# Optimization experiments

Hardware: AMD Instinct MI355X
Metric: run time of the kernel (lower is better)

## Reference

```python
import jax, jax.numpy as jnp
import numpy as np

B, C_IN, N_NODES = 128, 64, 1024
N_TRIPLES = 3 * (N_NODES - 1)  # node 0 is the shared zero vector


def _btc(x, idx, w, b):
    # x: [B, C, N]; idx: [B, 3M]; w: [O, C, 3]; b: [O]
    Bv, C, _ = x.shape
    T = idx.shape[1]
    g = jnp.take_along_axis(x, jnp.broadcast_to(idx[:, None, :], (Bv, C, T)), axis=2)
    g = g.reshape(Bv, C, T // 3, 3)  # stride-3 kernel-3 conv == per-triple contraction
    out = jnp.einsum('bcnk,ock->bon', g, w) + b[None, :, None]
    zero = jnp.zeros((Bv, out.shape[1], 1), dtype=out.dtype)
    return jnp.concatenate([zero, out], axis=2)  # re-prepend zero node -> [B, O, N]


def _tln(x):
    mean = jnp.mean(x, axis=(1, 2), keepdims=True)
    std = jnp.std(x, axis=(1, 2), ddof=1, keepdims=True)  # torch.std is unbiased
    return (x - mean) / (std + 1e-5)


def _tower(x, idx, p):
    x = jax.nn.leaky_relu(_tln(_btc(x, idx, p['w_conv1'], p['b_conv1'])), 0.01)
    x = jax.nn.leaky_relu(_tln(_btc(x, idx, p['w_conv2'], p['b_conv2'])), 0.01)
    x = _tln(_btc(x, idx, p['w_conv3'], p['b_conv3']))
    x = jnp.max(x, axis=2)  # DynamicPooling -> [B, 64]
    x = jax.nn.leaky_relu(x @ p['w_fc1'].T + p['b_fc1'], 0.01)
    return x @ p['w_fc2'].T + p['b_fc2']  # [B, 1]  (Dropout is identity at eval)


def setup_inputs() -> dict:
    key = jax.random.key(0)
    ks = jax.random.split(key, 12)
    s = 0.05
    return {
        'data1': jax.random.normal(ks[0], (B, C_IN, N_NODES), jnp.float32),
        'idx1': jax.random.randint(ks[1], (B, N_TRIPLES, 1), 0, N_NODES, dtype=jnp.int64)
                if jax.config.jax_enable_x64 else
                jax.random.randint(ks[1], (B, N_TRIPLES, 1), 0, N_NODES).astype(jnp.int32),
        'data2': jax.random.normal(ks[2], (B, C_IN, N_NODES), jnp.float32),
        'idx2': jax.random.randint(ks[3], (B, N_TRIPLES, 1), 0, N_NODES).astype(jnp.int32),
        'w_conv1': jax.random.normal(ks[4], (256, C_IN, 3), jnp.float32) * s,
        'b_conv1': jnp.zeros((256,), jnp.float32),
        'w_conv2': jax.random.normal(ks[5], (128, 256, 3), jnp.float32) * s,
        'b_conv2': jnp.zeros((128,), jnp.float32),
        'w_conv3': jax.random.normal(ks[6], (64, 128, 3), jnp.float32) * s,
        'b_conv3': jnp.zeros((64,), jnp.float32),
        'w_fc1': jax.random.normal(ks[7], (32, 64), jnp.float32) * s,
        'b_fc1': jnp.zeros((32,), jnp.float32),
        'w_fc2': jax.random.normal(ks[8], (1, 32), jnp.float32) * s,
        'b_fc2': jnp.zeros((1,), jnp.float32),
    }


def reference(data1, idx1, data2, idx2,
              w_conv1, b_conv1, w_conv2, b_conv2, w_conv3, b_conv3,
              w_fc1, b_fc1, w_fc2, b_fc2):
    p = dict(w_conv1=w_conv1, b_conv1=b_conv1, w_conv2=w_conv2, b_conv2=b_conv2,
             w_conv3=w_conv3, b_conv3=b_conv3, w_fc1=w_fc1, b_fc1=b_fc1,
             w_fc2=w_fc2, b_fc2=b_fc2)
    y1 = _tower(data1, idx1[..., 0], p)
    y2 = _tower(data2, idx2[..., 0], p)
    return jnp.squeeze(jax.nn.sigmoid(y1 - y2), axis=1)  # [B]
```

## Files before the change

### kernel.cpp

```cpp
#include <hip/hip_runtime.h>
#include <math.h>

typedef __attribute__((ext_vector_type(8))) short short8;
typedef __attribute__((ext_vector_type(4))) float f32x4;
typedef __attribute__((ext_vector_type(2))) float f32x2;

#define LRELU(x) ((x) > 0.0f ? (x) : 0.01f * (x))

struct __align__(4) Int3 { int x, y, z; };

__device__ __forceinline__ unsigned short f2bf(float f) {
    unsigned int u = __float_as_uint(f);
    return (unsigned short)((u + 0x7FFFu + ((u >> 16) & 1u)) >> 16);
}
__device__ __forceinline__ unsigned int pack_bf16_pair(float lo, float hi) {
    unsigned int ul = __float_as_uint(lo) + 0x8000u;
    unsigned int uh = __float_as_uint(hi) + 0x8000u;
    return (ul >> 16) | (uh & 0xFFFF0000u);
}
__device__ __forceinline__ float2 stats_from(const float* sums, int b, float count) {
    float s = sums[2 * b], q = sums[2 * b + 1];
    float mean = s / count;
    float var = (q - s * s / count) / (count - 1.0f);
    var = fmaxf(var, 0.0f);
    return make_float2(mean, 1.0f / (sqrtf(var) + 1e-5f));
}
__device__ __forceinline__ void atomicMaxF(float* a, float v) {
    if (v >= 0.0f) atomicMax((int*)a, __float_as_int(v));
    else           atomicMin((unsigned int*)a, __float_as_uint(v));
}
__device__ __forceinline__ unsigned int fp8x4_nact(unsigned int u, float a, float c) {
    f32x2 lo = __builtin_amdgcn_cvt_pk_f32_fp8(u, false);
    f32x2 hi = __builtin_amdgcn_cvt_pk_f32_fp8(u, true);
    lo = lo * a + c; hi = hi * a + c;
    f32x2 ml = lo * 0.01f, mh = hi * 0.01f;
    lo = __builtin_elementwise_max(lo, ml);
    hi = __builtin_elementwise_max(hi, mh);
    int r = __builtin_amdgcn_cvt_pk_fp8_f32(lo.x, lo.y, 0, false);
    r = __builtin_amdgcn_cvt_pk_fp8_f32(hi.x, hi.y, r, true);
    return (unsigned int)r;
}
__device__ __forceinline__ int perm128(int o) {
    return ((o >> 6) << 6) | (((o >> 3) & 3) << 4) | (((o >> 5) & 1) << 3) | (o & 7);
}

template <int MT, int WM>
__device__ __forceinline__ void mfma_step(const unsigned short* wt, const unsigned short* gt,
                                          f32x4 (&acc)[MT][4],
                                          int wo, int wn, int quad, int l15, int blkid)
{
#pragma unroll
    for (int st = 0; st < 2; ++st) {
        short8 af[MT], bfv[4];
        const int qb = st * 4 + quad;
#pragma unroll
        for (int i = 0; i < MT; i++) {
            const int orow = wo * WM + i * 16 + l15;
            af[i] = *(const short8*)&wt[orow * 64 + ((qb ^ blkid) << 3)];
        }
#pragma unroll
        for (int t = 0; t < 4; t++) {
            const int nrow = wn * 64 + t * 16 + l15;
            bfv[t] = *(const short8*)&gt[nrow * 64 + ((qb ^ blkid) << 3)];
        }
#pragma unroll
        for (int i = 0; i < MT; i++)
#pragma unroll
            for (int t = 0; t < 4; t++)
                acc[i][t] = __builtin_amdgcn_mfma_f32_16x16x32_bf16(
                    af[i], bfv[t], acc[i][t], 0, 0, 0);
    }
}

__global__ void prep_all(const float* __restrict__ w1, unsigned short* __restrict__ wq1,
                         const float* __restrict__ w2, unsigned char* __restrict__ wq2,
                         const float* __restrict__ w3, unsigned char* __restrict__ wq3)
{
    const int tid = blockIdx.x * blockDim.x + threadIdx.x;
    const int stride = gridDim.x * blockDim.x;
    for (int i = tid; i < 256 * 192; i += stride) {
        int o = i / 192, kp = i - o * 192;
        int j = kp >> 6, c = kp & 63;
        wq1[i] = f2bf(w1[(o * 64 + c) * 3 + j]);
    }
    for (int i = tid; i < (128 * 768) >> 2; i += stride) {
        const int e0 = i << 2;
        const int o = e0 / 768, r0 = e0 - o * 768;
        const int kc = r0 >> 7, ro = r0 & 127;
        const int k0 = ((ro >> 6) << 6) + (((ro >> 3) & 1) << 5) + (((ro >> 4) & 3) << 3) + (ro & 7);
        const int kp0 = kc * 128 + k0;
        const int j = kp0 >> 8, c0 = kp0 & 255;
        const float* src = &w2[(o * 256 + c0) * 3 + j];
        float f0 = src[0], f1 = src[3], f2 = src[6], f3 = src[9];
        int r = __builtin_amdgcn_cvt_pk_fp8_f32(f0, f1, 0, false);
        r = __builtin_amdgcn_cvt_pk_fp8_f32(f2, f3, r, true);
        *(unsigned int*)&wq2[e0] = (unsigned int)r;
    }
    for (int i = tid; i < (64 * 384) >> 2; i += stride) {
        const int e0 = i << 2;
        const int o = e0 / 384, r0 = e0 - o * 384;
        const int kc = r0 >> 7, ro = r0 & 127;
        const int k0 = ((ro >> 6) << 6) + (((ro >> 3) & 1) << 5) + (((ro >> 4) & 3) << 3) + (ro & 7);
        const int kp0 = kc * 128 + k0;
        const int j = kp0 >> 7, c0 = kp0 & 127;
        const float* src = &w3[(o * 128 + c0) * 3 + j];
        float f0 = src[0], f1 = src[3], f2 = src[6], f3 = src[9];
        int r = __builtin_amdgcn_cvt_pk_fp8_f32(f0, f1, 0, false);
        r = __builtin_amdgcn_cvt_pk_fp8_f32(f2, f3, r, true);
        *(unsigned int*)&wq3[e0] = (unsigned int)r;
    }
}

__global__ __launch_bounds__(256) void transpose_in(const float* __restrict__ inA,
                                                    const float* __restrict__ inB,
                                                    unsigned short* __restrict__ xT,
                                                    float* __restrict__ sums,
                                                    unsigned int* __restrict__ pmax)
{
    const int b = blockIdx.y, n0 = blockIdx.x * 64;
    const float* in = (b >= 128 ? inB : inA) + ((size_t)(b & 127) * 64) * 1024;
    const int tid = threadIdx.x;
    if (blockIdx.x == 0 && blockIdx.y == 0) {
        const int nBv = gridDim.y;
        for (int i = tid; i < 3 * nBv * 2; i += 256) sums[i] = 0.0f;
        for (int i = tid; i < nBv * 64; i += 256) pmax[i] = 0xFFFFFFFFu;
    }
    __shared__ float tile[64][65];
    const int nn = tid & 63, cw = tid >> 6;
#pragma unroll
    for (int i = 0; i < 16; i++) {
        int c = i * 4 + cw;
        tile[c][nn] = in[(size_t)c * 1024 + n0 + nn];
    }
    __syncthreads();
    const int n = tid >> 2, cp = (tid & 3) * 16;
    unsigned int pk[8];
#pragma unroll
    for (int i = 0; i < 8; i++) {
        unsigned short lo = f2bf(tile[cp + 2 * i][n]);
        unsigned short hi = f2bf(tile[cp + 2 * i + 1][n]);
        pk[i] = (unsigned int)lo | ((unsigned int)hi << 16);
    }
    unsigned short* dst = xT + ((size_t)b * 1024 + n0 + n) * 64 + cp;
    uint4 v0 = {pk[0], pk[1], pk[2], pk[3]};
    uint4 v1 = {pk[4], pk[5], pk[6], pk[7]};
    *(uint4*)dst = v0;
    *(uint4*)(dst + 8) = v1;
}

__global__ __launch_bounds__(256) void norm_act_fp8(unsigned char* __restrict__ a,
                                                    const float* __restrict__ sums,
                                                    float count, int u4PerB)
{
    const int b = blockIdx.y;
    float2 st = stats_from(sums, b, count);
    const float na = st.y, nc = -st.x * st.y;
    uint4* p = (uint4*)a + (size_t)b * u4PerB;
    for (int idx = blockIdx.x * 256 + threadIdx.x; idx < u4PerB; idx += gridDim.x * 256) {
        uint4 v = p[idx];
        v.x = fp8x4_nact(v.x, na, nc);
        v.y = fp8x4_nact(v.y, na, nc);
        v.z = fp8x4_nact(v.z, na, nc);
        v.w = fp8x4_nact(v.w, na, nc);
        p[idx] = v;
    }
}

__global__ __launch_bounds__(256, 3) void conv1_mfma(
    const unsigned short* __restrict__ xT,
    const int* __restrict__ idxA,
    const int* __restrict__ idxB,
    const unsigned short* __restrict__ wq,
    const float* __restrict__ bias,
    unsigned char* __restrict__ out,
    float* __restrict__ sums)
{
    const int b   = blockIdx.x;
    const int o0  = blockIdx.y * 128;
    const int nt0 = blockIdx.z << 7;
    const int tid = threadIdx.x;
    const int lane = tid & 63, wave = tid >> 6;
    const int wo = wave & 1, wn = wave >> 1;
    const int quad = lane >> 4, l15 = lane & 15;
    const int blkid = lane & 7;

    __shared__ __align__(16) unsigned short wt[128 * 64];
    __shared__ __align__(16) unsigned short gt[128 * 64];

    f32x4 acc[4][4];
#pragma unroll
    for (int i = 0; i < 4; i++)
#pragma unroll
        for (int t = 0; t < 4; t++) acc[i][t] = (f32x4){0.f, 0.f, 0.f, 0.f};

    const unsigned short* xTb = xT + (((size_t)b) << 10) * 64;
    const int* idxb = (b >= 128 ? idxB : idxA) + (size_t)(b & 127) * 3069;

    const int gr = tid >> 1, gh = tid & 1;
    int s0, s1, s2;
    {
        int n = nt0 + gr;
        int t0 = (n == 0) ? 0 : (n - 1);
        const Int3 sv = *(const Int3*)&idxb[3 * t0];
        s0 = sv.x; s1 = sv.y; s2 = sv.z;
    }
    const int wr = tid >> 1, wseg = tid & 1;
    const unsigned short* wrow = wq + (size_t)(o0 + wr) * 192 + wseg * 32;
    const int gswz = gr & 7, wswz = wr & 7;

    uint4 g0A, g1A, g2A, g3A;
    uint4 g0B, g1B, g2B, g3B;

#define LOADC(S, KC) {                                                           \
        const int src_ = ((KC) == 0) ? s0 : (((KC) == 1) ? s1 : s2);             \
        const uint4* gp_ = (const uint4*)(xTb + (size_t)src_ * 64 + gh * 32);    \
        g0##S = gp_[0]; g1##S = gp_[1]; g2##S = gp_[2]; g3##S = gp_[3];          \
    }

#define STAGE(S, KC) {                                                           \
        const uint4* wp_ = (const uint4*)(wrow + ((KC) << 6));                   \
        uint4 wv0 = wp_[0], wv1 = wp_[1], wv2 = wp_[2], wv3 = wp_[3];            \
        *(uint4*)&gt[gr * 64 + (((gh << 2) | 0) ^ gswz) * 8] = g0##S;            \
        *(uint4*)&gt[gr * 64 + (((gh << 2) | 1) ^ gswz) * 8] = g1##S;            \
        *(uint4*)&gt[gr * 64 + (((gh << 2) | 2) ^ gswz) * 8] = g2##S;            \
        *(uint4*)&gt[gr * 64 + (((gh << 2) | 3) ^ gswz) * 8] = g3##S;            \
        *(uint4*)&wt[wr * 64 + ((wseg * 4 + 0) ^ wswz) * 8] = wv0;               \
        *(uint4*)&wt[wr * 64 + ((wseg * 4 + 1) ^ wswz) * 8] = wv1;               \
        *(uint4*)&wt[wr * 64 + ((wseg * 4 + 2) ^ wswz) * 8] = wv2;               \
        *(uint4*)&wt[wr * 64 + ((wseg * 4 + 3) ^ wswz) * 8] = wv3;               \
    }

    LOADC(A, 0);
    LOADC(B, 1);
    int kc = 0;
    for (; kc + 2 <= 3; kc += 2) {
        if (kc) __syncthreads();
        STAGE(A, kc);
        if (kc + 2 < 3) LOADC(A, kc + 2);
        __syncthreads();
        mfma_step<4, 64>(wt, gt, acc, wo, wn, quad, l15, blkid);
        __syncthreads();
        STAGE(B, kc + 1);
        __syncthreads();
        mfma_step<4, 64>(wt, gt, acc, wo, wn, quad, l15, blkid);
    }
    {
        __syncthreads();
        STAGE(A, 2);
        __syncthreads();
        mfma_step<4, 64>(wt, gt, acc, wo, wn, quad, l15, blkid);
    }
#undef LOADC
#undef STAGE

    __syncthreads();
    unsigned char* eb = (unsigned char*)gt;
    float lsum = 0.f, lsq = 0.f;
#pragma unroll
    for (int i = 0; i < 4; i++) {
        const int obl = wo * 64 + i * 16 + quad * 4;
        const int op  = perm128(obl);
        const float4 bv = *(const float4*)(bias + o0 + obl);
#pragma unroll
        for (int t = 0; t < 4; t++) {
            const int nl = wn * 64 + t * 16 + l15;
            float v0 = acc[i][t][0] + bv.x;
            float v1 = acc[i][t][1] + bv.y;
            float v2 = acc[i][t][2] + bv.z;
            float v3 = acc[i][t][3] + bv.w;
            if (nt0 + nl == 0) { v0 = v1 = v2 = v3 = 0.f; }
            lsum += v0 + v1 + v2 + v3;
            lsq  += v0 * v0 + v1 * v1 + v2 * v2 + v3 * v3;
            int r = __builtin_amdgcn_cvt_pk_fp8_f32(v0, v1, 0, false);
            r = __builtin_amdgcn_cvt_pk_fp8_f32(v2, v3, r, true);
            *(unsigned int*)&eb[nl * 128 + (op ^ ((nl & 7) << 4))] = (unsigned int)r;
        }
    }
#pragma unroll
    for (int off = 32; off > 0; off >>= 1) {
        lsum += __shfl_down(lsum, off);
        lsq  += __shfl_down(lsq, off);
    }
    float* red = (float*)wt;
    if (lane == 0) { red[wave] = lsum; red[4 + wave] = lsq; }
    __syncthreads();
#pragma unroll
    for (int c = 0; c < 4; ++c) {
        const int ch = c * 256 + tid;
        const int row = ch >> 3, off = (ch & 7) << 4;
        uint4 v = *(const uint4*)&eb[row * 128 + (off ^ ((row & 7) << 4))];
        *(uint4*)&out[((size_t)b * 1024 + nt0 + row) * 256 + o0 + off] = v;
    }
    if (tid == 0) {
        atomicAdd(&sums[2 * b + 0], red[0] + red[1] + red[2] + red[3]);
        atomicAdd(&sums[2 * b + 1], red[4] + red[5] + red[6] + red[7]);
    }
}

__global__ __launch_bounds__(256, 3) void conv2_fp8(
    const unsigned char* __restrict__ a1,
    const int* __restrict__ idxA,
    const int* __restrict__ idxB,
    const unsigned char* __restrict__ wq8,
    const float* __restrict__ bias,
    unsigned char* __restrict__ out,
    float* __restrict__ sums)
{
    const int b   = blockIdx.x;
    const int nt0 = blockIdx.z << 7;
    const int tid = threadIdx.x;
    const int lane = tid & 63, wave = tid >> 6;
    const int wo = wave & 1, wn = wave >> 1;
    const int quad = lane >> 4, l15 = lane & 15;
    const int blkid = lane & 7;

    __shared__ __align__(16) unsigned char wt8[128 * 128];
    __shared__ __align__(16) unsigned char gt8[128 * 128];

    f32x4 acc[4][4];
#pragma unroll
    for (int i = 0; i < 4; i++)
#pragma unroll
        for (int t = 0; t < 4; t++) acc[i][t] = (f32x4){0.f, 0.f, 0.f, 0.f};

    const unsigned char* xb = a1 + (((size_t)b) << 10) * 256;
    const int* idxb = (b >= 128 ? idxB : idxA) + (size_t)(b & 127) * 3069;

    const int gr = tid >> 1, gh = tid & 1;
    int si0, si1, si2;
    {
        int n = nt0 + gr;
        int t0 = (n == 0) ? 0 : (n - 1);
        const Int3 sv = *(const Int3*)&idxb[3 * t0];
        si0 = sv.x; si1 = sv.y; si2 = sv.z;
    }
    const unsigned char* wrow = wq8 + (size_t)gr * 768 + gh * 64;
    const int swz = gr & 7;

    uint4 g0A, g1A, g2A, g3A;
    uint4 g0B, g1B, g2B, g3B;

#define LOADC2(S, KC) {                                                          \
        const int j_  = (KC) >> 1;                                               \
        const int c0_ = ((KC) & 1) << 7;                                         \
        const int src_ = (j_ == 0) ? si0 : ((j_ == 1) ? si1 : si2);              \
        const uint4* gp_ = (const uint4*)(xb + (size_t)src_ * 256 + c0_ + gh * 64); \
        g0##S = gp_[0]; g1##S = gp_[1]; g2##S = gp_[2]; g3##S = gp_[3];          \
    }

#define STAGE2(S, KC) {                                                          \
        const uint4* wp_ = (const uint4*)(wrow + (KC) * 128);                    \
        uint4 wv0 = wp_[0], wv1 = wp_[1], wv2 = wp_[2], wv3 = wp_[3];            \
        *(uint4*)&gt8[gr * 128 + (((gh << 2) | 0) ^ swz) * 16] = g0##S;          \
        *(uint4*)&gt8[gr * 128 + (((gh << 2) | 1) ^ swz) * 16] = g1##S;          \
        *(uint4*)&gt8[gr * 128 + (((gh << 2) | 2) ^ swz) * 16] = g2##S;          \
        *(uint4*)&gt8[gr * 128 + (((gh << 2) | 3) ^ swz) * 16] = g3##S;          \
        *(uint4*)&wt8[gr * 128 + (((gh << 2) | 0) ^ swz) * 16] = wv0;            \
        *(uint4*)&wt8[gr * 128 + (((gh << 2) | 1) ^ swz) * 16] = wv1;            \
        *(uint4*)&wt8[gr * 128 + (((gh << 2) | 2) ^ swz) * 16] = wv2;            \
        *(uint4*)&wt8[gr * 128 + (((gh << 2) | 3) ^ swz) * 16] = wv3;            \
    }

#define MFMA_STEP2 {                                                             \
        _Pragma("unroll")                                                        \
        for (int pp = 0; pp < 2; ++pp) {                                         \
            ulonglong2 a0v, a1v, a2v, a3v, b0v, b1v, b2v, b3v;                   \
            {                                                                    \
                const int cx = (((pp * 4 + quad) ^ blkid) << 4);                 \
                a0v = *(const ulonglong2*)&wt8[(wo * 64 +  0 + l15) * 128 + cx]; \
                a1v = *(const ulonglong2*)&wt8[(wo * 64 + 16 + l15) * 128 + cx]; \
                a2v = *(const ulonglong2*)&wt8[(wo * 64 + 32 + l15) * 128 + cx]; \
                a3v = *(const ulonglong2*)&wt8[(wo * 64 + 48 + l15) * 128 + cx]; \
                b0v = *(const ulonglong2*)&gt8[(wn * 64 +  0 + l15) * 128 + cx]; \
                b1v = *(const ulonglong2*)&gt8[(wn * 64 + 16 + l15) * 128 + cx]; \
                b2v = *(const ulonglong2*)&gt8[(wn * 64 + 32 + l15) * 128 + cx]; \
                b3v = *(const ulonglong2*)&gt8[(wn * 64 + 48 + l15) * 128 + cx]; \
            }                                                                    \
            acc[0][0] = __builtin_amdgcn_mfma_f32_16x16x32_fp8_fp8((long)a0v.x, (long)b0v.x, acc[0][0], 0, 0, 0); \
            acc[0][1] = __builtin_amdgcn_mfma_f32_16x16x32_fp8_fp8((long)a0v.x, (long)b1v.x, acc[0][1], 0, 0, 0); \
            acc[0][2] = __builtin_amdgcn_mfma_f32_16x16x32_fp8_fp8((long)a0v.x, (long)b2v.x, acc[0][2], 0, 0, 0); \
            acc[0][3] = __builtin_amdgcn_mfma_f32_16x16x32_fp8_fp8((long)a0v.x, (long)b3v.x, acc[0][3], 0, 0, 0); \
            acc[1][0] = __builtin_amdgcn_mfma_f32_16x16x32_fp8_fp8((long)a1v.x, (long)b0v.x, acc[1][0], 0, 0, 0); \
            acc[1][1] = __builtin_amdgcn_mfma_f32_16x16x32_fp8_fp8((long)a1v.x, (long)b1v.x, acc[1][1], 0, 0, 0); \
            acc[1][2] = __builtin_amdgcn_mfma_f32_16x16x32_fp8_fp8((long)a1v.x, (long)b2v.x, acc[1][2], 0, 0, 0); \
            acc[1][3] = __builtin_amdgcn_mfma_f32_16x16x32_fp8_fp8((long)a1v.x, (long)b3v.x, acc[1][3], 0, 0, 0); \
            acc[2][0] = __builtin_amdgcn_mfma_f32_16x16x32_fp8_fp8((long)a2v.x, (long)b0v.x, acc[2][0], 0, 0, 0); \
            acc[2][1] = __builtin_amdgcn_mfma_f32_16x16x32_fp8_fp8((long)a2v.x, (long)b1v.x, acc[2][1], 0, 0, 0); \
            acc[2][2] = __builtin_amdgcn_mfma_f32_16x16x32_fp8_fp8((long)a2v.x, (long)b2v.x, acc[2][2], 0, 0, 0); \
            acc[2][3] = __builtin_amdgcn_mfma_f32_16x16x32_fp8_fp8((long)a2v.x, (long)b3v.x, acc[2][3], 0, 0, 0); \
            acc[3][0] = __builtin_amdgcn_mfma_f32_16x16x32_fp8_fp8((long)a3v.x, (long)b0v.x, acc[3][0], 0, 0, 0); \
            acc[3][1] = __builtin_amdgcn_mfma_f32_16x16x32_fp8_fp8((long)a3v.x, (long)b1v.x, acc[3][1], 0, 0, 0); \
            acc[3][2] = __builtin_amdgcn_mfma_f32_16x16x32_fp8_fp8((long)a3v.x, (long)b2v.x, acc[3][2], 0, 0, 0); \
            acc[3][3] = __builtin_amdgcn_mfma_f32_16x16x32_fp8_fp8((long)a3v.x, (long)b3v.x, acc[3][3], 0, 0, 0); \
            acc[0][0] = __builtin_amdgcn_mfma_f32_16x16x32_fp8_fp8((long)a0v.y, (long)b0v.y, acc[0][0], 0, 0, 0); \
            acc[0][1] = __builtin_amdgcn_mfma_f32_16x16x32_fp8_fp8((long)a0v.y, (long)b1v.y, acc[0][1], 0, 0, 0); \
            acc[0][2] = __builtin_amdgcn_mfma_f32_16x16x32_fp8_fp8((long)a0v.y, (long)b2v.y, acc[0][2], 0, 0, 0); \
            acc[0][3] = __builtin_amdgcn_mfma_f32_16x16x32_fp8_fp8((long)a0v.y, (long)b3v.y, acc[0][3], 0, 0, 0); \
            acc[1][0] = __builtin_amdgcn_mfma_f32_16x16x32_fp8_fp8((long)a1v.y, (long)b0v.y, acc[1][0], 0, 0, 0); \
            acc[1][1] = __builtin_amdgcn_mfma_f32_16x16x32_fp8_fp8((long)a1v.y, (long)b1v.y, acc[1][1], 0, 0, 0); \
            acc[1][2] = __builtin_amdgcn_mfma_f32_16x16x32_fp8_fp8((long)a1v.y, (long)b2v.y, acc[1][2], 0, 0, 0); \
            acc[1][3] = __builtin_amdgcn_mfma_f32_16x16x32_fp8_fp8((long)a1v.y, (long)b3v.y, acc[1][3], 0, 0, 0); \
            acc[2][0] = __builtin_amdgcn_mfma_f32_16x16x32_fp8_fp8((long)a2v.y, (long)b0v.y, acc[2][0], 0, 0, 0); \
            acc[2][1] = __builtin_amdgcn_mfma_f32_16x16x32_fp8_fp8((long)a2v.y, (long)b1v.y, acc[2][1], 0, 0, 0); \
            acc[2][2] = __builtin_amdgcn_mfma_f32_16x16x32_fp8_fp8((long)a2v.y, (long)b2v.y, acc[2][2], 0, 0, 0); \
            acc[2][3] = __builtin_amdgcn_mfma_f32_16x16x32_fp8_fp8((long)a2v.y, (long)b3v.y, acc[2][3], 0, 0, 0); \
            acc[3][0] = __builtin_amdgcn_mfma_f32_16x16x32_fp8_fp8((long)a3v.y, (long)b0v.y, acc[3][0], 0, 0, 0); \
            acc[3][1] = __builtin_amdgcn_mfma_f32_16x16x32_fp8_fp8((long)a3v.y, (long)b1v.y, acc[3][1], 0, 0, 0); \
            acc[3][2] = __builtin_amdgcn_mfma_f32_16x16x32_fp8_fp8((long)a3v.y, (long)b2v.y, acc[3][2], 0, 0, 0); \
            acc[3][3] = __builtin_amdgcn_mfma_f32_16x16x32_fp8_fp8((long)a3v.y, (long)b3v.y, acc[3][3], 0, 0, 0); \
        }                                                                        \
    }

    LOADC2(A, 0);
    LOADC2(B, 1);
    int kc = 0;
    for (; kc + 2 <= 6; kc += 2) {
        if (kc) __syncthreads();
        STAGE2(A, kc);
        if (kc + 2 < 6) LOADC2(A, kc + 2);
        __syncthreads();
        MFMA_STEP2;
        __syncthreads();
        STAGE2(B, kc + 1);
        if (kc + 3 < 6) LOADC2(B, kc + 3);
        __syncthreads();
        MFMA_STEP2;
    }
#undef LOADC2
#undef STAGE2
#undef MFMA_STEP2

    __syncthreads();
    unsigned char* eb = gt8;
    float lsum = 0.f, lsq = 0.f;
#pragma unroll
    for (int i = 0; i < 4; i++) {
        const int obl = wo * 64 + i * 16 + quad * 4;
        const int op  = perm128(obl);
        const float4 bv = *(const float4*)(bias + obl);
#pragma unroll
        for (int t = 0; t < 4; t++) {
            const int nl = wn * 64 + t * 16 + l15;
            float v0 = acc[i][t][0] + bv.x;
            float v1 = acc[i][t][1] + bv.y;
            float v2 = acc[i][t][2] + bv.z;
            float v3 = acc[i][t][3] + bv.w;
            if (nt0 + nl == 0) { v0 = v1 = v2 = v3 = 0.f; }
            lsum += v0 + v1 + v2 + v3;
            lsq  += v0 * v0 + v1 * v1 + v2 * v2 + v3 * v3;
            int r = __builtin_amdgcn_cvt_pk_fp8_f32(v0, v1, 0, false);
            r = __builtin_amdgcn_cvt_pk_fp8_f32(v2, v3, r, true);
            *(unsigned int*)&eb[nl * 128 + (op ^ ((nl & 7) << 4))] = (unsigned int)r;
        }
    }
#pragma unroll
    for (int off = 32; off > 0; off >>= 1) {
        lsum += __shfl_down(lsum, off);
        lsq  += __shfl_down(lsq, off);
    }
    float* red = (float*)wt8;
    if (lane == 0) { red[wave] = lsum; red[4 + wave] = lsq; }
    __syncthreads();
#pragma unroll
    for (int c = 0; c < 4; ++c) {
        const int ch = c * 256 + tid;
        const int row = ch >> 3, off = (ch & 7) << 4;
        uint4 v = *(const uint4*)&eb[row * 128 + (off ^ ((row & 7) << 4))];
        *(uint4*)&out[((size_t)b * 1024 + nt0 + row) * 128 + off] = v;
    }
    if (tid == 0) {
        atomicAdd(&sums[2 * b + 0], red[0] + red[1] + red[2] + red[3]);
        atomicAdd(&sums[2 * b + 1], red[4] + red[5] + red[6] + red[7]);
    }
}

__global__ __launch_bounds__(256, 3) void conv3_fp8(
    const unsigned char* __restrict__ a2,
    const int* __restrict__ idxA,
    const int* __restrict__ idxB,
    const unsigned char* __restrict__ wq8,
    const float* __restrict__ bias,
    float* __restrict__ sums,
    float* __restrict__ pmax)
{
    const int b   = blockIdx.x;
    const int nt0 = blockIdx.z << 7;
    const int tid = threadIdx.x;
    const int lane = tid & 63, wave = tid >> 6;
    const int wo = wave & 1, wn = wave >> 1;
    const int quad = lane >> 4, l15 = lane & 15;
    const int blkid = lane & 7;

    __shared__ __align__(16) unsigned char wt8[64 * 128];
    __shared__ __align__(16) unsigned char gt8[128 * 128];

    f32x4 acc[2][4];
#pragma unroll
    for (int i = 0; i < 2; i++)
#pragma unroll
        for (int t = 0; t < 4; t++) acc[i][t] = (f32x4){0.f, 0.f, 0.f, 0.f};

    const unsigned char* xb = a2 + (((size_t)b) << 10) * 128;
    const int* idxb = (b >= 128 ? idxB : idxA) + (size_t)(b & 127) * 3069;

    const int gr = tid >> 1, gh = tid & 1;
    int si0, si1, si2;
    {
        int n = nt0 + gr;
        int t0 = (n == 0) ? 0 : (n - 1);
        const Int3 sv = *(const Int3*)&idxb[3 * t0];
        si0 = sv.x; si1 = sv.y; si2 = sv.z;
    }
    const int wr = tid >> 2, wseg = tid & 3;
    const unsigned char* wrow = wq8 + (size_t)wr * 384 + wseg * 32;
    const int gswz = gr & 7, wswz = wr & 7;

    uint4 g0A, g1A, g2A, g3A;
    uint4 g0B, g1B, g2B, g3B;

#define LOADC3(S, KC) {                                                          \
        const int src_ = ((KC) == 0) ? si0 : (((KC) == 1) ? si1 : si2);          \
        const uint4* gp_ = (const uint4*)(xb + (size_t)src_ * 128 + gh * 64);    \
        g0##S = gp_[0]; g1##S = gp_[1]; g2##S = gp_[2]; g3##S = gp_[3];          \
    }

#define STAGE3(S, KC) {                                                          \
        const uint4* wp_ = (const uint4*)(wrow + (KC) * 128);                    \
        uint4 wv0 = wp_[0], wv1 = wp_[1];                                        \
        *(uint4*)&gt8[gr * 128 + (((gh << 2) | 0) ^ gswz) * 16] = g0##S;         \
        *(uint4*)&gt8[gr * 128 + (((gh << 2) | 1) ^ gswz) * 16] = g1##S;         \
        *(uint4*)&gt8[gr * 128 + (((gh << 2) | 2) ^ gswz) * 16] = g2##S;         \
        *(uint4*)&gt8[gr * 128 + (((gh << 2) | 3) ^ gswz) * 16] = g3##S;         \
        *(uint4*)&wt8[wr * 128 + (((wseg << 1) | 0) ^ wswz) * 16] = wv0;         \
        *(uint4*)&wt8[wr * 128 + (((wseg << 1) | 1) ^ wswz) * 16] = wv1;         \
    }

#define MFMA_STEP3 {                                                             \
        _Pragma("unroll")                                                        \
        for (int pp = 0; pp < 2; ++pp) {                                         \
            ulonglong2 a0v, a1v, b0v, b1v, b2v, b3v;                             \
            {                                                                    \
                const int cx = (((pp * 4 + quad) ^ blkid) << 4);                 \
                a0v = *(const ulonglong2*)&wt8[(wo * 32 +  0 + l15) * 128 + cx]; \
                a1v = *(const ulonglong2*)&wt8[(wo * 32 + 16 + l15) * 128 + cx]; \
                b0v = *(const ulonglong2*)&gt8[(wn * 64 +  0 + l15) * 128 + cx]; \
                b1v = *(const ulonglong2*)&gt8[(wn * 64 + 16 + l15) * 128 + cx]; \
                b2v = *(const ulonglong2*)&gt8[(wn * 64 + 32 + l15) * 128 + cx]; \
                b3v = *(const ulonglong2*)&gt8[(wn * 64 + 48 + l15) * 128 + cx]; \
            }                                                                    \
            acc[0][0] = __builtin_amdgcn_mfma_f32_16x16x32_fp8_fp8((long)a0v.x, (long)b0v.x, acc[0][0], 0, 0, 0); \
            acc[0][1] = __builtin_amdgcn_mfma_f32_16x16x32_fp8_fp8((long)a0v.x, (long)b1v.x, acc[0][1], 0, 0, 0); \
            acc[0][2] = __builtin_amdgcn_mfma_f32_16x16x32_fp8_fp8((long)a0v.x, (long)b2v.x, acc[0][2], 0, 0, 0); \
            acc[0][3] = __builtin_amdgcn_mfma_f32_16x16x32_fp8_fp8((long)a0v.x, (long)b3v.x, acc[0][3], 0, 0, 0); \
            acc[1][0] = __builtin_amdgcn_mfma_f32_16x16x32_fp8_fp8((long)a1v.x, (long)b0v.x, acc[1][0], 0, 0, 0); \
            acc[1][1] = __builtin_amdgcn_mfma_f32_16x16x32_fp8_fp8((long)a1v.x, (long)b1v.x, acc[1][1], 0, 0, 0); \
            acc[1][2] = __builtin_amdgcn_mfma_f32_16x16x32_fp8_fp8((long)a1v.x, (long)b2v.x, acc[1][2], 0, 0, 0); \
            acc[1][3] = __builtin_amdgcn_mfma_f32_16x16x32_fp8_fp8((long)a1v.x, (long)b3v.x, acc[1][3], 0, 0, 0); \
            acc[0][0] = __builtin_amdgcn_mfma_f32_16x16x32_fp8_fp8((long)a0v.y, (long)b0v.y, acc[0][0], 0, 0, 0); \
            acc[0][1] = __builtin_amdgcn_mfma_f32_16x16x32_fp8_fp8((long)a0v.y, (long)b1v.y, acc[0][1], 0, 0, 0); \
            acc[0][2] = __builtin_amdgcn_mfma_f32_16x16x32_fp8_fp8((long)a0v.y, (long)b2v.y, acc[0][2], 0, 0, 0); \
            acc[0][3] = __builtin_amdgcn_mfma_f32_16x16x32_fp8_fp8((long)a0v.y, (long)b3v.y, acc[0][3], 0, 0, 0); \
            acc[1][0] = __builtin_amdgcn_mfma_f32_16x16x32_fp8_fp8((long)a1v.y, (long)b0v.y, acc[1][0], 0, 0, 0); \
            acc[1][1] = __builtin_amdgcn_mfma_f32_16x16x32_fp8_fp8((long)a1v.y, (long)b1v.y, acc[1][1], 0, 0, 0); \
            acc[1][2] = __builtin_amdgcn_mfma_f32_16x16x32_fp8_fp8((long)a1v.y, (long)b2v.y, acc[1][2], 0, 0, 0); \
            acc[1][3] = __builtin_amdgcn_mfma_f32_16x16x32_fp8_fp8((long)a1v.y, (long)b3v.y, acc[1][3], 0, 0, 0); \
        }                                                                        \
    }

    LOADC3(A, 0);
    LOADC3(B, 1);
    int kc = 0;
    for (; kc + 2 <= 3; kc += 2) {
        if (kc) __syncthreads();
        STAGE3(A, kc);
        if (kc + 2 < 3) LOADC3(A, kc + 2);
        __syncthreads();
        MFMA_STEP3;
        __syncthreads();
        STAGE3(B, kc + 1);
        __syncthreads();
        MFMA_STEP3;
    }
    {
        __syncthreads();
        STAGE3(A, 2);
        __syncthreads();
        MFMA_STEP3;
    }
#undef LOADC3
#undef STAGE3
#undef MFMA_STEP3

    __syncthreads();
    float lsum = 0.f, lsq = 0.f;
#pragma unroll
    for (int i = 0; i < 2; i++) {
        const int ob = wo * 32 + i * 16 + quad * 4;
        const float4 bv = *(const float4*)(bias + ob);
        float mx0 = -1e30f, mx1 = -1e30f, mx2 = -1e30f, mx3 = -1e30f;
#pragma unroll
        for (int t = 0; t < 4; t++) {
            const int n = nt0 + wn * 64 + t * 16 + l15;
            float v0 = acc[i][t][0] + bv.x;
            float v1 = acc[i][t][1] + bv.y;
            float v2 = acc[i][t][2] + bv.z;
            float v3 = acc[i][t][3] + bv.w;
            if (n == 0) { v0 = v1 = v2 = v3 = 0.f; }
            lsum += v0 + v1 + v2 + v3;
            lsq  += v0 * v0 + v1 * v1 + v2 * v2 + v3 * v3;
            mx0 = fmaxf(mx0, v0); mx1 = fmaxf(mx1, v1);
            mx2 = fmaxf(mx2, v2); mx3 = fmaxf(mx3, v3);
        }
#pragma unroll
        for (int off = 1; off < 16; off <<= 1) {
            mx0 = fmaxf(mx0, __shfl_xor(mx0, off));
            mx1 = fmaxf(mx1, __shfl_xor(mx1, off));
            mx2 = fmaxf(mx2, __shfl_xor(mx2, off));
            mx3 = fmaxf(mx3, __shfl_xor(mx3, off));
        }
        if (l15 == 0) {
            atomicMaxF(&pmax[(size_t)b * 64 + ob + 0], mx0);
            atomicMaxF(&pmax[(size_t)b * 64 + ob + 1], mx1);
            atomicMaxF(&pmax[(size_t)b * 64 + ob + 2], mx2);
            atomicMaxF(&pmax[(size_t)b * 64 + ob + 3], mx3);
        }
    }
#pragma unroll
    for (int off = 32; off > 0; off >>= 1) {
        lsum += __shfl_down(lsum, off);
        lsq  += __shfl_down(lsq, off);
    }
    float* red = (float*)wt8;
    if (lane == 0) { red[wave] = lsum; red[4 + wave] = lsq; }
    __syncthreads();
    if (tid == 0) {
        atomicAdd(&sums[2 * b + 0], red[0] + red[1] + red[2] + red[3]);
        atomicAdd(&sums[2 * b + 1], red[4] + red[5] + red[6] + red[7]);
    }
}

__global__ __launch_bounds__(64) void fc_head(
    const float* __restrict__ pmax, const float* __restrict__ sums3, float count,
    const float* __restrict__ w_fc1, const float* __restrict__ b_fc1,
    const float* __restrict__ w_fc2, const float* __restrict__ b_fc2,
    float* __restrict__ y)
{
    const int b = blockIdx.x, t = threadIdx.x;
    __shared__ float pooled[64];
    __shared__ float hid[32];
    float2 s = stats_from(sums3, b, count);
    pooled[t] = (pmax[(size_t)b * 64 + t] - s.x) * s.y;
    __syncthreads();
    if (t < 32) {
        float h = b_fc1[t];
#pragma unroll
        for (int c = 0; c < 64; c++) h += pooled[c] * w_fc1[t * 64 + c];
        hid[t] = LRELU(h);
    }
    __syncthreads();
    if (t == 0) {
        float v = b_fc2[0];
#pragma unroll
        for (int c = 0; c < 32; c++) v += hid[c] * w_fc2[c];
        y[b] = v;
    }
}

__global__ void sigmoid_diff(const float* __restrict__ y1,
                             const float* __restrict__ y2,
                             float* __restrict__ out)
{
    int b = threadIdx.x;
    if (b < 128) out[b] = 1.0f / (1.0f + expf(-(y1[b] - y2[b])));
}

extern "C" void kernel_launch(void* const* d_in, const int* in_sizes, int n_in,
                              void* d_out, int out_size, void* d_ws, size_t ws_size,
                              hipStream_t stream)
{
    const float* data1 = (const float*)d_in[0];
    const int*   idx1  = (const int*)d_in[1];
    const float* data2 = (const float*)d_in[2];
    const int*   idx2  = (const int*)d_in[3];
    const float* w1 = (const float*)d_in[4];
    const float* b1 = (const float*)d_in[5];
    const float* w2 = (const float*)d_in[6];
    const float* b2 = (const float*)d_in[7];
    const float* w3 = (const float*)d_in[8];
    const float* b3 = (const float*)d_in[9];
    const float* wfc1 = (const float*)d_in[10];
    const float* bfc1 = (const float*)d_in[11];
    const float* wfc2 = (const float*)d_in[12];
    const float* bfc2 = (const float*)d_in[13];

    const size_t needM = (size_t)256 * 1024 * (64 * 2 + 256 * 1 + 128 * 1) + 768 * 1024;
    const bool merged = ws_size >= needM;
    const int nB = merged ? 256 : 128;
    const size_t szXT = (size_t)nB * 1024 * 64 * 2;
    const size_t szA1 = (size_t)nB * 1024 * 256;
    const size_t szA2 = (size_t)nB * 1024 * 128;

    char* ws = (char*)d_ws;
    unsigned short* xT = (unsigned short*)ws;
    unsigned char*  a1 = (unsigned char*)(ws + szXT);
    unsigned char*  a2 = (unsigned char*)(ws + szXT + szA1);
    char* tail = ws + szXT + szA1 + szA2;
    unsigned short* wq1   = (unsigned short*)tail;
    unsigned char*  wq2f8 = (unsigned char*)(tail + 128 * 1024);
    unsigned char*  wq3f8 = (unsigned char*)(tail + 384 * 1024);
    float* sums = (float*)(tail + 448 * 1024);
    float* pmax = (float*)(tail + 512 * 1024);
    float* yv   = (float*)(tail + 640 * 1024);

    prep_all<<<96, 256, 0, stream>>>(w1, wq1, w2, wq2f8, w3, wq3f8);

    const int nIter = merged ? 1 : 2;
    for (int t = 0; t < nIter; ++t) {
        const float* dA = (merged || t == 0) ? data1 : data2;
        const float* dB = merged ? data2 : dA;
        const int* iA = (merged || t == 0) ? idx1 : idx2;
        const int* iB = merged ? idx2 : iA;
        float* s1 = sums;
        float* s2 = sums + nB * 2;
        float* s3 = sums + nB * 4;

        transpose_in<<<dim3(16, nB), 256, 0, stream>>>(dA, dB, xT, sums,
                                                       (unsigned int*)pmax);

        conv1_mfma<<<dim3(nB, 2, 8), 256, 0, stream>>>(
            xT, iA, iB, wq1, b1, a1, s1);

        norm_act_fp8<<<dim3(16, nB), 256, 0, stream>>>(a1, s1, 256.0f * 1024.0f, 16384);

        conv2_fp8<<<dim3(nB, 1, 8), 256, 0, stream>>>(
            a1, iA, iB, wq2f8, b2, a2, s2);

        norm_act_fp8<<<dim3(8, nB), 256, 0, stream>>>(a2, s2, 128.0f * 1024.0f, 8192);

        conv3_fp8<<<dim3(nB, 1, 8), 256, 0, stream>>>(
            a2, iA, iB, wq3f8, b3, s3, pmax);

        fc_head<<<nB, 64, 0, stream>>>(pmax, s3, 64.0f * 1024.0f,
                                       wfc1, bfc1, wfc2, bfc2,
                                       yv + (merged ? 0 : t * 128));
    }
    sigmoid_diff<<<1, 128, 0, stream>>>(yv, yv + 128, (float*)d_out);
}
```

Baseline: 269.5 us.

## Enlarge conv workgroups to 512 threads with bigger output tiles

All three conv kernels now run 8-wave, 512-thread blocks. conv1 covers all 256 output channels per block instead of splitting across blockIdx.y, so each gathered input tile is loaded once. conv2 and conv3 now cover 256 nodes per block instead of 128, so each weight tile is reused over twice as many nodes. The aim is to cut redundant gather and weight traffic and block count, at the cost of more LDS per block, fewer blocks (less parallelism for small grids) and reworked staging and epilogue index maps.

```diff
diff --git a/kernel.cpp b/kernel.cpp
--- a/kernel.cpp
+++ b/kernel.cpp
@@ -166,7 +166,7 @@
     }
 }
 
-__global__ __launch_bounds__(256, 3) void conv1_mfma(
+__global__ __launch_bounds__(512, 2) void conv1_mfma(
     const unsigned short* __restrict__ xT,
     const int* __restrict__ idxA,
     const int* __restrict__ idxB,
@@ -176,15 +176,14 @@
     float* __restrict__ sums)
 {
     const int b   = blockIdx.x;
-    const int o0  = blockIdx.y * 128;
     const int nt0 = blockIdx.z << 7;
     const int tid = threadIdx.x;
     const int lane = tid & 63, wave = tid >> 6;
-    const int wo = wave & 1, wn = wave >> 1;
+    const int wo = wave & 3, wn = wave >> 2;
     const int quad = lane >> 4, l15 = lane & 15;
     const int blkid = lane & 7;
 
-    __shared__ __align__(16) unsigned short wt[128 * 64];
+    __shared__ __align__(16) unsigned short wt[256 * 64];
     __shared__ __align__(16) unsigned short gt[128 * 64];
 
     f32x4 acc[4][4];
@@ -196,7 +195,7 @@
     const unsigned short* xTb = xT + (((size_t)b) << 10) * 64;
     const int* idxb = (b >= 128 ? idxB : idxA) + (size_t)(b & 127) * 3069;
 
-    const int gr = tid >> 1, gh = tid & 1;
+    const int gr = tid >> 2, gh = tid & 3;
     int s0, s1, s2;
     {
         int n = nt0 + gr;
@@ -205,25 +204,22 @@
         s0 = sv.x; s1 = sv.y; s2 = sv.z;
     }
     const int wr = tid >> 1, wseg = tid & 1;
-    const unsigned short* wrow = wq + (size_t)(o0 + wr) * 192 + wseg * 32;
+    const unsigned short* wrow = wq + (size_t)wr * 192 + wseg * 32;
     const int gswz = gr & 7, wswz = wr & 7;
 
-    uint4 g0A, g1A, g2A, g3A;
-    uint4 g0B, g1B, g2B, g3B;
+    uint4 g0A, g1A, g0B, g1B;
 
 #define LOADC(S, KC) {                                                           \
         const int src_ = ((KC) == 0) ? s0 : (((KC) == 1) ? s1 : s2);             \
-        const uint4* gp_ = (const uint4*)(xTb + (size_t)src_ * 64 + gh * 32);    \
-        g0##S = gp_[0]; g1##S = gp_[1]; g2##S = gp_[2]; g3##S = gp_[3];          \
+        const uint4* gp_ = (const uint4*)(xTb + (size_t)src_ * 64 + gh * 16);    \
+        g0##S = gp_[0]; g1##S = gp_[1];                                          \
     }
 
 #define STAGE(S, KC) {                                                           \
         const uint4* wp_ = (const uint4*)(wrow + ((KC) << 6));                   \
         uint4 wv0 = wp_[0], wv1 = wp_[1], wv2 = wp_[2], wv3 = wp_[3];            \
-        *(uint4*)&gt[gr * 64 + (((gh << 2) | 0) ^ gswz) * 8] = g0##S;            \
-        *(uint4*)&gt[gr * 64 + (((gh << 2) | 1) ^ gswz) * 8] = g1##S;            \
-        *(uint4*)&gt[gr * 64 + (((gh << 2) | 2) ^ gswz) * 8] = g2##S;            \
-        *(uint4*)&gt[gr * 64 + (((gh << 2) | 3) ^ gswz) * 8] = g3##S;            \
+        *(uint4*)&gt[gr * 64 + (((gh << 1) | 0) ^ gswz) * 8] = g0##S;            \
+        *(uint4*)&gt[gr * 64 + (((gh << 1) | 1) ^ gswz) * 8] = g1##S;            \
         *(uint4*)&wt[wr * 64 + ((wseg * 4 + 0) ^ wswz) * 8] = wv0;               \
         *(uint4*)&wt[wr * 64 + ((wseg * 4 + 1) ^ wswz) * 8] = wv1;               \
         *(uint4*)&wt[wr * 64 + ((wseg * 4 + 2) ^ wswz) * 8] = wv2;               \
@@ -254,13 +250,13 @@
 #undef STAGE
 
     __syncthreads();
-    unsigned char* eb = (unsigned char*)gt;
+    unsigned char* eb = (unsigned char*)wt;
     float lsum = 0.f, lsq = 0.f;
 #pragma unroll
     for (int i = 0; i < 4; i++) {
         const int obl = wo * 64 + i * 16 + quad * 4;
         const int op  = perm128(obl);
-        const float4 bv = *(const float4*)(bias + o0 + obl);
+        const float4 bv = *(const float4*)(bias + obl);
 #pragma unroll
         for (int t = 0; t < 4; t++) {
             const int nl = wn * 64 + t * 16 + l15;
@@ -273,7 +269,7 @@
             lsq  += v0 * v0 + v1 * v1 + v2 * v2 + v3 * v3;
             int r = __builtin_amdgcn_cvt_pk_fp8_f32(v0, v1, 0, false);
             r = __builtin_amdgcn_cvt_pk_fp8_f32(v2, v3, r, true);
-            *(unsigned int*)&eb[nl * 128 + (op ^ ((nl & 7) << 4))] = (unsigned int)r;
+            *(unsigned int*)&eb[nl * 256 + (op ^ ((nl & 7) << 4))] = (unsigned int)r;
         }
     }
 #pragma unroll
@@ -281,23 +277,28 @@
         lsum += __shfl_down(lsum, off);
         lsq  += __shfl_down(lsq, off);
     }
-    float* red = (float*)wt;
-    if (lane == 0) { red[wave] = lsum; red[4 + wave] = lsq; }
-    __syncthreads();
-#pragma unroll
-    for (int c = 0; c < 4; ++c) {
-        const int ch = c * 256 + tid;
-        const int row = ch >> 3, off = (ch & 7) << 4;
-        uint4 v = *(const uint4*)&eb[row * 128 + (off ^ ((row & 7) << 4))];
-        *(uint4*)&out[((size_t)b * 1024 + nt0 + row) * 256 + o0 + off] = v;
+    float* red = (float*)gt;
+    if (lane == 0) { red[wave] = lsum; red[8 + wave] = lsq; }
+    __syncthreads();
+    {
+        const int row = tid >> 2, c0 = (tid & 3) * 64;
+#pragma unroll
+        for (int i = 0; i < 4; ++i) {
+            const int off = c0 + i * 16;
+            uint4 v = *(const uint4*)&eb[row * 256 + (off ^ ((row & 7) << 4))];
+            *(uint4*)&out[((size_t)b * 1024 + nt0 + row) * 256 + off] = v;
+        }
     }
     if (tid == 0) {
-        atomicAdd(&sums[2 * b + 0], red[0] + red[1] + red[2] + red[3]);
-        atomicAdd(&sums[2 * b + 1], red[4] + red[5] + red[6] + red[7]);
-    }
-}
-
-__global__ __launch_bounds__(256, 3) void conv2_fp8(
+        float a0 = 0.f, a1 = 0.f;
+#pragma unroll
+        for (int w = 0; w < 8; ++w) { a0 += red[w]; a1 += red[8 + w]; }
+        atomicAdd(&sums[2 * b + 0], a0);
+        atomicAdd(&sums[2 * b + 1], a1);
+    }
+}
+
+__global__ __launch_bounds__(512, 2) void conv2_fp8(
     const unsigned char* __restrict__ a1,
     const int* __restrict__ idxA,
     const int* __restrict__ idxB,
@@ -307,7 +308,7 @@
     float* __restrict__ sums)
 {
     const int b   = blockIdx.x;
-    const int nt0 = blockIdx.z << 7;
+    const int nt0 = blockIdx.z << 8;
     const int tid = threadIdx.x;
     const int lane = tid & 63, wave = tid >> 6;
     const int wo = wave & 1, wn = wave >> 1;
@@ -315,7 +316,7 @@
     const int blkid = lane & 7;
 
     __shared__ __align__(16) unsigned char wt8[128 * 128];
-    __shared__ __align__(16) unsigned char gt8[128 * 128];
+    __shared__ __align__(16) unsigned char gt8[256 * 128];
 
     f32x4 acc[4][4];
 #pragma unroll
@@ -334,8 +335,9 @@
         const Int3 sv = *(const Int3*)&idxb[3 * t0];
         si0 = sv.x; si1 = sv.y; si2 = sv.z;
     }
-    const unsigned char* wrow = wq8 + (size_t)gr * 768 + gh * 64;
-    const int swz = gr & 7;
+    const int wr = tid >> 2, wseg = tid & 3;
+    const unsigned char* wrow = wq8 + (size_t)wr * 768 + wseg * 32;
+    const int gswz = gr & 7, wswz = wr & 7;
 
     uint4 g0A, g1A, g2A, g3A;
     uint4 g0B, g1B, g2B, g3B;
@@ -350,15 +352,13 @@
 
 #define STAGE2(S, KC) {                                                          \
         const uint4* wp_ = (const uint4*)(wrow + (KC) * 128);                    \
-        uint4 wv0 = wp_[0], wv1 = wp_[1], wv2 = wp_[2], wv3 = wp_[3];            \
-        *(uint4*)&gt8[gr * 128 + (((gh << 2) | 0) ^ swz) * 16] = g0##S;          \
-        *(uint4*)&gt8[gr * 128 + (((gh << 2) | 1) ^ swz) * 16] = g1##S;          \
-        *(uint4*)&gt8[gr * 128 + (((gh << 2) | 2) ^ swz) * 16] = g2##S;          \
-        *(uint4*)&gt8[gr * 128 + (((gh << 2) | 3) ^ swz) * 16] = g3##S;          \
-        *(uint4*)&wt8[gr * 128 + (((gh << 2) | 0) ^ swz) * 16] = wv0;            \
-        *(uint4*)&wt8[gr * 128 + (((gh << 2) | 1) ^ swz) * 16] = wv1;            \
-        *(uint4*)&wt8[gr * 128 + (((gh << 2) | 2) ^ swz) * 16] = wv2;            \
-        *(uint4*)&wt8[gr * 128 + (((gh << 2) | 3) ^ swz) * 16] = wv3;            \
+        uint4 wv0 = wp_[0], wv1 = wp_[1];                                        \
+        *(uint4*)&gt8[gr * 128 + (((gh << 2) | 0) ^ gswz) * 16] = g0##S;         \
+        *(uint4*)&gt8[gr * 128 + (((gh << 2) | 1) ^ gswz) * 16] = g1##S;         \
+        *(uint4*)&gt8[gr * 128 + (((gh << 2) | 2) ^ gswz) * 16] = g2##S;         \
+        *(uint4*)&gt8[gr * 128 + (((gh << 2) | 3) ^ gswz) * 16] = g3##S;         \
+        *(uint4*)&wt8[wr * 128 + (((wseg << 1) | 0) ^ wswz) * 16] = wv0;         \
+        *(uint4*)&wt8[wr * 128 + (((wseg << 1) | 1) ^ wswz) * 16] = wv1;         \
     }
 
 #define MFMA_STEP2 {                                                             \
@@ -459,22 +459,27 @@
         lsq  += __shfl_down(lsq, off);
     }
     float* red = (float*)wt8;
-    if (lane == 0) { red[wave] = lsum; red[4 + wave] = lsq; }
-    __syncthreads();
-#pragma unroll
-    for (int c = 0; c < 4; ++c) {
-        const int ch = c * 256 + tid;
-        const int row = ch >> 3, off = (ch & 7) << 4;
-        uint4 v = *(const uint4*)&eb[row * 128 + (off ^ ((row & 7) << 4))];
-        *(uint4*)&out[((size_t)b * 1024 + nt0 + row) * 128 + off] = v;
+    if (lane == 0) { red[wave] = lsum; red[8 + wave] = lsq; }
+    __syncthreads();
+    {
+        const int row = tid >> 1, c0 = (tid & 1) * 64;
+#pragma unroll
+        for (int i = 0; i < 4; ++i) {
+            const int off = c0 + i * 16;
+            uint4 v = *(const uint4*)&eb[row * 128 + (off ^ ((row & 7) << 4))];
+            *(uint4*)&out[((size_t)b * 1024 + nt0 + row) * 128 + off] = v;
+        }
     }
     if (tid == 0) {
-        atomicAdd(&sums[2 * b + 0], red[0] + red[1] + red[2] + red[3]);
-        atomicAdd(&sums[2 * b + 1], red[4] + red[5] + red[6] + red[7]);
-    }
-}
-
-__global__ __launch_bounds__(256, 3) void conv3_fp8(
+        float a0 = 0.f, a1v = 0.f;
+#pragma unroll
+        for (int w = 0; w < 8; ++w) { a0 += red[w]; a1v += red[8 + w]; }
+        atomicAdd(&sums[2 * b + 0], a0);
+        atomicAdd(&sums[2 * b + 1], a1v);
+    }
+}
+
+__global__ __launch_bounds__(512, 2) void conv3_fp8(
     const unsigned char* __restrict__ a2,
     const int* __restrict__ idxA,
     const int* __restrict__ idxB,
@@ -484,7 +489,7 @@
     float* __restrict__ pmax)
 {
     const int b   = blockIdx.x;
-    const int nt0 = blockIdx.z << 7;
+    const int nt0 = blockIdx.z << 8;
     const int tid = threadIdx.x;
     const int lane = tid & 63, wave = tid >> 6;
     const int wo = wave & 1, wn = wave >> 1;
@@ -492,7 +497,7 @@
     const int blkid = lane & 7;
 
     __shared__ __align__(16) unsigned char wt8[64 * 128];
-    __shared__ __align__(16) unsigned char gt8[128 * 128];
+    __shared__ __align__(16) unsigned char gt8[256 * 128];
 
     f32x4 acc[2][4];
 #pragma unroll
@@ -511,8 +516,8 @@
         const Int3 sv = *(const Int3*)&idxb[3 * t0];
         si0 = sv.x; si1 = sv.y; si2 = sv.z;
     }
-    const int wr = tid >> 2, wseg = tid & 3;
-    const unsigned char* wrow = wq8 + (size_t)wr * 384 + wseg * 32;
+    const int wr = tid >> 3, wseg = tid & 7;
+    const unsigned char* wrow = wq8 + (size_t)wr * 384 + wseg * 16;
     const int gswz = gr & 7, wswz = wr & 7;
 
     uint4 g0A, g1A, g2A, g3A;
@@ -525,14 +530,12 @@
     }
 
 #define STAGE3(S, KC) {                                                          \
-        const uint4* wp_ = (const uint4*)(wrow + (KC) * 128);                    \
-        uint4 wv0 = wp_[0], wv1 = wp_[1];                                        \
+        uint4 wv0 = *(const uint4*)(wrow + (KC) * 128);                          \
         *(uint4*)&gt8[gr * 128 + (((gh << 2) | 0) ^ gswz) * 16] = g0##S;         \
         *(uint4*)&gt8[gr * 128 + (((gh << 2) | 1) ^ gswz) * 16] = g1##S;         \
         *(uint4*)&gt8[gr * 128 + (((gh << 2) | 2) ^ gswz) * 16] = g2##S;         \
         *(uint4*)&gt8[gr * 128 + (((gh << 2) | 3) ^ gswz) * 16] = g3##S;         \
-        *(uint4*)&wt8[wr * 128 + (((wseg << 1) | 0) ^ wswz) * 16] = wv0;         \
-        *(uint4*)&wt8[wr * 128 + (((wseg << 1) | 1) ^ wswz) * 16] = wv1;         \
+        *(uint4*)&wt8[wr * 128 + (wseg ^ wswz) * 16] = wv0;                      \
     }
 
 #define MFMA_STEP3 {                                                             \
@@ -631,11 +634,14 @@
         lsq  += __shfl_down(lsq, off);
     }
     float* red = (float*)wt8;
-    if (lane == 0) { red[wave] = lsum; red[4 + wave] = lsq; }
+    if (lane == 0) { red[wave] = lsum; red[8 + wave] = lsq; }
     __syncthreads();
     if (tid == 0) {
-        atomicAdd(&sums[2 * b + 0], red[0] + red[1] + red[2] + red[3]);
-        atomicAdd(&sums[2 * b + 1], red[4] + red[5] + red[6] + red[7]);
+        float a0 = 0.f, a1v = 0.f;
+#pragma unroll
+        for (int w = 0; w < 8; ++w) { a0 += red[w]; a1v += red[8 + w]; }
+        atomicAdd(&sums[2 * b + 0], a0);
+        atomicAdd(&sums[2 * b + 1], a1v);
     }
 }
 
@@ -727,17 +733,17 @@
         transpose_in<<<dim3(16, nB), 256, 0, stream>>>(dA, dB, xT, sums,
                                                        (unsigned int*)pmax);
 
-        conv1_mfma<<<dim3(nB, 2, 8), 256, 0, stream>>>(
+        conv1_mfma<<<dim3(nB, 1, 8), 512, 0, stream>>>(
             xT, iA, iB, wq1, b1, a1, s1);
 
         norm_act_fp8<<<dim3(16, nB), 256, 0, stream>>>(a1, s1, 256.0f * 1024.0f, 16384);
 
-        conv2_fp8<<<dim3(nB, 1, 8), 256, 0, stream>>>(
+        conv2_fp8<<<dim3(nB, 1, 4), 512, 0, stream>>>(
             a1, iA, iB, wq2f8, b2, a2, s2);
 
         norm_act_fp8<<<dim3(8, nB), 256, 0, stream>>>(a2, s2, 128.0f * 1024.0f, 8192);
 
-        conv3_fp8<<<dim3(nB, 1, 8), 256, 0, stream>>>(
+        conv3_fp8<<<dim3(nB, 1, 4), 512, 0, stream>>>(
             a2, iA, iB, wq3f8, b3, s3, pmax);
 
         fc_head<<<nB, 64, 0, stream>>>(pmax, s3, 64.0f * 1024.0f,
```

Result: slower. 308.5 us (+14.5%).
